# Performance work log

Measured on AMD Instinct MI355X. Metric: run time of the kernel, lower is better.

The kernel has to match this reference:

```python
import jax, jax.numpy as jnp
import numpy as np

N_NODES = 100000
N_EDGES = 1600000
IN_F = 256
OUT_F = 64


def setup_inputs() -> dict:
    key = jax.random.key(0)
    k1, k2, k3, k4, k5, k6 = jax.random.split(key, 6)
    x = jax.random.normal(k1, (N_NODES, IN_F), dtype=jnp.float32)
    edge_vals = jax.random.uniform(k2, (N_EDGES,), dtype=jnp.float32)
    W = jax.random.normal(k3, (IN_F, OUT_F), dtype=jnp.float32) * (1.0 / np.sqrt(OUT_F))
    bias = jax.random.normal(k4, (OUT_F,), dtype=jnp.float32) * (1.0 / np.sqrt(OUT_F))
    row_idx = jnp.sort(jax.random.randint(k5, (N_EDGES,), 0, N_NODES, dtype=jnp.int32))
    col_idx = jax.random.randint(k6, (N_EDGES,), 0, N_NODES, dtype=jnp.int32)
    return {"x": x, "edge_vals": edge_vals, "W": W, "bias": bias,
            "row_idx": row_idx, "col_idx": col_idx}


def reference(x, edge_vals, W, bias, row_idx, col_idx):
    # support = X @ W  (dense GEMM; torch.mm / torch.spmm branch)
    support = x @ W                                  # [N, OUT_F]
    # flexspmm: output = A @ support, A given as weighted edge list
    msgs = support[col_idx] * edge_vals[:, None]      # [E, OUT_F] gather + scale
    out = jax.ops.segment_sum(msgs, row_idx, num_segments=x.shape[0])  # [N, OUT_F]
    return out + bias
```

## Files before the change

kernel.cpp:

```cpp
#include <hip/hip_runtime.h>
#include <hip/hip_bf16.h>

#define N_NODES 100000
#define N_EDGES 1600000
#define IN_F 256
#define OUT_F 64

typedef short bf16x8 __attribute__((ext_vector_type(8)));
typedef float f32x4 __attribute__((ext_vector_type(4)));
typedef unsigned short u16x8 __attribute__((ext_vector_type(8)));

__device__ __forceinline__ short f2bf(float f) {
  unsigned u = __float_as_uint(f);
  u += 0x7FFF + ((u >> 16) & 1);
  return (short)(u >> 16);
}
__device__ __forceinline__ float bf2f(unsigned short u) {
  return __uint_as_float(((unsigned)u) << 16);
}

__global__ __launch_bounds__(256) void build_row_ptr_kernel(
    const int* __restrict__ row_idx, int* __restrict__ row_ptr) {
  int i = blockIdx.x * blockDim.x + threadIdx.x;
  if (i > N_NODES) return;
  int lo = 0, hi = N_EDGES;
  while (lo < hi) {
    int mid = (lo + hi) >> 1;
    if (row_idx[mid] < i) lo = mid + 1; else hi = mid;
  }
  row_ptr[i] = lo;
}

__global__ __launch_bounds__(256) void wfrag_kernel(
    const float* __restrict__ W, short* __restrict__ Wf) {
  int tid = blockIdx.x * blockDim.x + threadIdx.x;
  if (tid >= 2048) return;
  int s = tid >> 8;
  int r = tid & 255;
  int t = r >> 6;
  int lane = r & 63;
  int col = t * 16 + (lane & 15);
  int kbase = s * 32 + ((lane >> 4) & 3) * 8;
#pragma unroll
  for (int j = 0; j < 8; ++j) {
    Wf[(size_t)tid * 8 + j] = f2bf(W[(size_t)(kbase + j) * OUT_F + col]);
  }
}

__global__ __launch_bounds__(256) void gemm_kernel(
    const float* __restrict__ x, const short* __restrict__ Wf,
    unsigned short* __restrict__ supB) {
  __shared__ short sWf[8 * 4 * 64 * 8];
  {
    const float4* g = reinterpret_cast<const float4*>(Wf);
    float4* s4 = reinterpret_cast<float4*>(sWf);
#pragma unroll
    for (int i = 0; i < 8; ++i) s4[threadIdx.x + i * 256] = g[threadIdx.x + i * 256];
  }
  __syncthreads();

  const int lane = threadIdx.x & 63;
  const int wave = threadIdx.x >> 6;
  const int r0_base = blockIdx.x * 64 + wave * 16;

  int arow = r0_base + (lane & 15);
  if (arow >= N_NODES) arow = N_NODES - 1;
  const float* xrow = x + (size_t)arow * IN_F + ((lane >> 4) & 3) * 8;

  f32x4 acc0 = {0.f, 0.f, 0.f, 0.f};
  f32x4 acc1 = {0.f, 0.f, 0.f, 0.f};
  f32x4 acc2 = {0.f, 0.f, 0.f, 0.f};
  f32x4 acc3 = {0.f, 0.f, 0.f, 0.f};

#pragma unroll
  for (int s = 0; s < 8; ++s) {
    const float4 f0 = *reinterpret_cast<const float4*>(xrow + s * 32);
    const float4 f1 = *reinterpret_cast<const float4*>(xrow + s * 32 + 4);
    bf16x8 a;
    a[0] = f2bf(f0.x); a[1] = f2bf(f0.y); a[2] = f2bf(f0.z); a[3] = f2bf(f0.w);
    a[4] = f2bf(f1.x); a[5] = f2bf(f1.y); a[6] = f2bf(f1.z); a[7] = f2bf(f1.w);
    const bf16x8 b0 = *reinterpret_cast<const bf16x8*>(&sWf[((s * 4 + 0) * 64 + lane) * 8]);
    const bf16x8 b1 = *reinterpret_cast<const bf16x8*>(&sWf[((s * 4 + 1) * 64 + lane) * 8]);
    const bf16x8 b2 = *reinterpret_cast<const bf16x8*>(&sWf[((s * 4 + 2) * 64 + lane) * 8]);
    const bf16x8 b3 = *reinterpret_cast<const bf16x8*>(&sWf[((s * 4 + 3) * 64 + lane) * 8]);
    acc0 = __builtin_amdgcn_mfma_f32_16x16x32_bf16(a, b0, acc0, 0, 0, 0);
    acc1 = __builtin_amdgcn_mfma_f32_16x16x32_bf16(a, b1, acc1, 0, 0, 0);
    acc2 = __builtin_amdgcn_mfma_f32_16x16x32_bf16(a, b2, acc2, 0, 0, 0);
    acc3 = __builtin_amdgcn_mfma_f32_16x16x32_bf16(a, b3, acc3, 0, 0, 0);
  }

  const int orow_base = r0_base + ((lane >> 4) & 3) * 4;
  const int ocol = lane & 15;
#pragma unroll
  for (int r = 0; r < 4; ++r) {
    const int row = orow_base + r;
    if (row < N_NODES) {
      unsigned short* o = supB + (size_t)row * OUT_F + ocol;
      o[0]  = (unsigned short)f2bf(acc0[r]);
      o[16] = (unsigned short)f2bf(acc1[r]);
      o[32] = (unsigned short)f2bf(acc2[r]);
      o[48] = (unsigned short)f2bf(acc3[r]);
    }
  }
}

__global__ __launch_bounds__(256) void spmm_kernel(
    const unsigned short* __restrict__ supB, const float* __restrict__ ev,
    const int* __restrict__ col, const int* __restrict__ row_ptr,
    const float* __restrict__ bias, float* __restrict__ out) {
  const int lane = threadIdx.x & 63;
  const int g = lane >> 3;
  const int fo = lane & 7;
  const int gwave = (blockIdx.x * blockDim.x + threadIdx.x) >> 6;
  const int nwaves = (gridDim.x * blockDim.x) >> 6;

  float b[8];
#pragma unroll
  for (int j = 0; j < 8; ++j) b[j] = bias[fo * 8 + j];

  for (int node = gwave; node < N_NODES; node += nwaves) {
    const int s = row_ptr[node];
    const int e = row_ptr[node + 1];
    float acc[8] = {0.f, 0.f, 0.f, 0.f, 0.f, 0.f, 0.f, 0.f};

    for (int i = s; i < e; i += 16) {
      const int i0 = i + g;
      const int i1 = i + 8 + g;
      const bool p0 = i0 < e;
      const bool p1 = i1 < e;
      const int c0 = col[p0 ? i0 : s];
      const int c1 = col[p1 ? i1 : s];
      const float v0 = p0 ? ev[i0] : 0.f;
      const float v1 = p1 ? ev[i1] : 0.f;
      const u16x8 s0 = *reinterpret_cast<const u16x8*>(supB + (size_t)c0 * OUT_F + fo * 8);
      const u16x8 s1 = *reinterpret_cast<const u16x8*>(supB + (size_t)c1 * OUT_F + fo * 8);
#pragma unroll
      for (int j = 0; j < 8; ++j) acc[j] = fmaf(v0, bf2f(s0[j]), acc[j]);
#pragma unroll
      for (int j = 0; j < 8; ++j) acc[j] = fmaf(v1, bf2f(s1[j]), acc[j]);
    }

#pragma unroll
    for (int j = 0; j < 8; ++j) {
      acc[j] += __shfl_xor(acc[j], 8);
      acc[j] += __shfl_xor(acc[j], 16);
      acc[j] += __shfl_xor(acc[j], 32);
    }

    if (lane < 8) {
      f32x4 oA = {acc[0] + b[0], acc[1] + b[1], acc[2] + b[2], acc[3] + b[3]};
      f32x4 oB = {acc[4] + b[4], acc[5] + b[5], acc[6] + b[6], acc[7] + b[7]};
      float* o = out + (size_t)node * OUT_F + fo * 8;
      *reinterpret_cast<f32x4*>(o) = oA;
      *reinterpret_cast<f32x4*>(o + 4) = oB;
    }
  }
}

extern "C" void kernel_launch(void* const* d_in, const int* in_sizes, int n_in,
                              void* d_out, int out_size, void* d_ws, size_t ws_size,
                              hipStream_t stream) {
  const float* x        = (const float*)d_in[0];
  const float* ev       = (const float*)d_in[1];
  const float* W        = (const float*)d_in[2];
  const float* bias     = (const float*)d_in[3];
  const int*   row_idx  = (const int*)d_in[4];
  const int*   col_idx  = (const int*)d_in[5];
  float* out = (float*)d_out;

  int*            row_ptr = (int*)d_ws;
  short*          Wf      = (short*)((char*)d_ws + 448 * 1024);
  unsigned short* supB    = (unsigned short*)((char*)d_ws + 512 * 1024);

  build_row_ptr_kernel<<<(N_NODES + 1 + 255) / 256, 256, 0, stream>>>(row_idx, row_ptr);
  wfrag_kernel<<<8, 256, 0, stream>>>(W, Wf);

  gemm_kernel<<<(N_NODES + 63) / 64, 256, 0, stream>>>(x, Wf, supB);

  spmm_kernel<<<2048, 256, 0, stream>>>(supB, ev, col_idx, row_ptr, bias, out);
}
```

Before: 71.39 us.

## Merge prep kernels and software-pipeline SpMM with contiguous node ranges

Merges the row_ptr binary search and the W fragment conversion into a single launch, so one kernel launch is removed. The SpMM kernel now gives each wave a contiguous range of nodes instead of a strided set, and prefetches the next chunk's column indices and edge values while the current chunk's gathers run. This targets index-load latency and per-node loop overhead. The cost is more complex control flow, and load imbalance is possible if the per-node degrees within a range vary.

```diff
diff --git a/kernel.cpp b/kernel.cpp
--- a/kernel.cpp
+++ b/kernel.cpp
@@ -19,31 +19,31 @@
   return __uint_as_float(((unsigned)u) << 16);
 }
 
-__global__ __launch_bounds__(256) void build_row_ptr_kernel(
-    const int* __restrict__ row_idx, int* __restrict__ row_ptr) {
-  int i = blockIdx.x * blockDim.x + threadIdx.x;
-  if (i > N_NODES) return;
-  int lo = 0, hi = N_EDGES;
-  while (lo < hi) {
-    int mid = (lo + hi) >> 1;
-    if (row_idx[mid] < i) lo = mid + 1; else hi = mid;
-  }
-  row_ptr[i] = lo;
-}
-
-__global__ __launch_bounds__(256) void wfrag_kernel(
+__global__ __launch_bounds__(256) void prep_kernel(
+    const int* __restrict__ row_idx, int* __restrict__ row_ptr,
     const float* __restrict__ W, short* __restrict__ Wf) {
-  int tid = blockIdx.x * blockDim.x + threadIdx.x;
-  if (tid >= 2048) return;
-  int s = tid >> 8;
-  int r = tid & 255;
-  int t = r >> 6;
-  int lane = r & 63;
-  int col = t * 16 + (lane & 15);
-  int kbase = s * 32 + ((lane >> 4) & 3) * 8;
-#pragma unroll
-  for (int j = 0; j < 8; ++j) {
-    Wf[(size_t)tid * 8 + j] = f2bf(W[(size_t)(kbase + j) * OUT_F + col]);
+  const int b = blockIdx.x;
+  if (b < 392) {
+    int i = b * 256 + threadIdx.x;
+    if (i > N_NODES) return;
+    int lo = 0, hi = N_EDGES;
+    while (lo < hi) {
+      int mid = (lo + hi) >> 1;
+      if (row_idx[mid] < i) lo = mid + 1; else hi = mid;
+    }
+    row_ptr[i] = lo;
+  } else {
+    int tid = (b - 392) * 256 + threadIdx.x;
+    int s = tid >> 8;
+    int r = tid & 255;
+    int t = r >> 6;
+    int lane = r & 63;
+    int col = t * 16 + (lane & 15);
+    int kbase = s * 32 + ((lane >> 4) & 3) * 8;
+#pragma unroll
+    for (int j = 0; j < 8; ++j) {
+      Wf[(size_t)tid * 8 + j] = f2bf(W[(size_t)(kbase + j) * OUT_F + col]);
+    }
   }
 }
 
@@ -114,46 +114,77 @@
   const int gwave = (blockIdx.x * blockDim.x + threadIdx.x) >> 6;
   const int nwaves = (gridDim.x * blockDim.x) >> 6;
 
+  const int per = (N_NODES + nwaves - 1) / nwaves;
+  const int n0 = gwave * per;
+  if (n0 >= N_NODES) return;
+  const int n1 = (n0 + per < N_NODES) ? n0 + per : N_NODES;
+
   float b[8];
 #pragma unroll
   for (int j = 0; j < 8; ++j) b[j] = bias[fo * 8 + j];
 
-  for (int node = gwave; node < N_NODES; node += nwaves) {
-    const int s = row_ptr[node];
-    const int e = row_ptr[node + 1];
-    float acc[8] = {0.f, 0.f, 0.f, 0.f, 0.f, 0.f, 0.f, 0.f};
-
-    for (int i = s; i < e; i += 16) {
-      const int i0 = i + g;
-      const int i1 = i + 8 + g;
-      const bool p0 = i0 < e;
-      const bool p1 = i1 < e;
-      const int c0 = col[p0 ? i0 : s];
-      const int c1 = col[p1 ? i1 : s];
-      const float v0 = p0 ? ev[i0] : 0.f;
-      const float v1 = p1 ? ev[i1] : 0.f;
-      const u16x8 s0 = *reinterpret_cast<const u16x8*>(supB + (size_t)c0 * OUT_F + fo * 8);
-      const u16x8 s1 = *reinterpret_cast<const u16x8*>(supB + (size_t)c1 * OUT_F + fo * 8);
-#pragma unroll
-      for (int j = 0; j < 8; ++j) acc[j] = fmaf(v0, bf2f(s0[j]), acc[j]);
-#pragma unroll
-      for (int j = 0; j < 8; ++j) acc[j] = fmaf(v1, bf2f(s1[j]), acc[j]);
-    }
-
-#pragma unroll
-    for (int j = 0; j < 8; ++j) {
-      acc[j] += __shfl_xor(acc[j], 8);
-      acc[j] += __shfl_xor(acc[j], 16);
-      acc[j] += __shfl_xor(acc[j], 32);
-    }
-
-    if (lane < 8) {
-      f32x4 oA = {acc[0] + b[0], acc[1] + b[1], acc[2] + b[2], acc[3] + b[3]};
-      f32x4 oB = {acc[4] + b[4], acc[5] + b[5], acc[6] + b[6], acc[7] + b[7]};
-      float* o = out + (size_t)node * OUT_F + fo * 8;
-      *reinterpret_cast<f32x4*>(o) = oA;
-      *reinterpret_cast<f32x4*>(o + 4) = oB;
-    }
+  int n = n0;
+  int i = row_ptr[n0];
+  int eCur = row_ptr[n0 + 1];
+  int eNext = row_ptr[(n0 + 2 <= N_NODES) ? n0 + 2 : N_NODES];
+
+  int pos0 = i + g, pos1 = i + 8 + g;
+  int cp0 = pos0 < N_EDGES ? pos0 : N_EDGES - 1;
+  int cp1 = pos1 < N_EDGES ? pos1 : N_EDGES - 1;
+  int   c0 = col[cp0];
+  int   c1 = col[cp1];
+  float v0 = ev[cp0];
+  float v1 = ev[cp1];
+
+  float acc[8] = {0.f, 0.f, 0.f, 0.f, 0.f, 0.f, 0.f, 0.f};
+
+  while (true) {
+    const bool more = (i + 16 < eCur);
+    const int ni = more ? (i + 16) : eCur;
+
+    const int np0 = ni + g, np1 = ni + 8 + g;
+    const int ncp0 = np0 < N_EDGES ? np0 : N_EDGES - 1;
+    const int ncp1 = np1 < N_EDGES ? np1 : N_EDGES - 1;
+    const int   nc0 = col[ncp0];
+    const int   nc1 = col[ncp1];
+    const float nv0 = ev[ncp0];
+    const float nv1 = ev[ncp1];
+
+    const float u0 = (pos0 < eCur) ? v0 : 0.f;
+    const float u1 = (pos1 < eCur) ? v1 : 0.f;
+    const u16x8 s0 = *reinterpret_cast<const u16x8*>(supB + (size_t)c0 * OUT_F + fo * 8);
+    const u16x8 s1 = *reinterpret_cast<const u16x8*>(supB + (size_t)c1 * OUT_F + fo * 8);
+#pragma unroll
+    for (int j = 0; j < 8; ++j) acc[j] = fmaf(u0, bf2f(s0[j]), acc[j]);
+#pragma unroll
+    for (int j = 0; j < 8; ++j) acc[j] = fmaf(u1, bf2f(s1[j]), acc[j]);
+
+    if (!more) {
+#pragma unroll
+      for (int j = 0; j < 8; ++j) {
+        acc[j] += __shfl_xor(acc[j], 8);
+        acc[j] += __shfl_xor(acc[j], 16);
+        acc[j] += __shfl_xor(acc[j], 32);
+      }
+      if (lane < 8) {
+        float* o = out + (size_t)n * OUT_F + fo * 8;
+        f32x4 oA = {acc[0] + b[0], acc[1] + b[1], acc[2] + b[2], acc[3] + b[3]};
+        f32x4 oB = {acc[4] + b[4], acc[5] + b[5], acc[6] + b[6], acc[7] + b[7]};
+        *reinterpret_cast<f32x4*>(o) = oA;
+        *reinterpret_cast<f32x4*>(o + 4) = oB;
+      }
+      ++n;
+      if (n >= n1) break;
+#pragma unroll
+      for (int j = 0; j < 8; ++j) acc[j] = 0.f;
+      eCur = eNext;
+      eNext = row_ptr[(n + 2 <= N_NODES) ? n + 2 : N_NODES];
+    }
+
+    i = ni;
+    pos0 = np0; pos1 = np1;
+    c0 = nc0; c1 = nc1;
+    v0 = nv0; v1 = nv1;
   }
 }
 
@@ -172,8 +203,7 @@
   short*          Wf      = (short*)((char*)d_ws + 448 * 1024);
   unsigned short* supB    = (unsigned short*)((char*)d_ws + 512 * 1024);
 
-  build_row_ptr_kernel<<<(N_NODES + 1 + 255) / 256, 256, 0, stream>>>(row_idx, row_ptr);
-  wfrag_kernel<<<8, 256, 0, stream>>>(W, Wf);
+  prep_kernel<<<400, 256, 0, stream>>>(row_idx, row_ptr, W, Wf);
 
   gemm_kernel<<<(N_NODES + 63) / 64, 256, 0, stream>>>(x, Wf, supB);
 
```

Result: no change. 70.20 us (-1.7%).
